# Optimization experiments

Measured on AMD Instinct MI355X. Metric: run time of the kernel, lower is better.

The kernel has to match this reference:

```python
import jax, jax.numpy as jnp
import numpy as np

D_MODEL = 1024
NUM_HEAD = 16
LN_EPS = 1e-5


def _layernorm(x, w, b):
    mu = jnp.mean(x, axis=-1, keepdims=True)
    var = jnp.mean(jnp.square(x - mu), axis=-1, keepdims=True)
    return (x - mu) * jax.lax.rsqrt(var + LN_EPS) * w + b


def setup_inputs() -> dict:
    key = jax.random.key(0)
    ks = jax.random.split(key, 8)
    d = D_MODEL
    s = 1.0 / np.sqrt(d)
    return {
        "text": jax.random.normal(ks[0], (8, 512, d), dtype=jnp.float32),
        "av_feat": jax.random.normal(ks[1], (8, 1024, d), dtype=jnp.float32),
        "tn_w": jnp.ones((d,), jnp.float32),
        "tn_b": jnp.zeros((d,), jnp.float32),
        "an_w": jnp.ones((d,), jnp.float32),
        "an_b": jnp.zeros((d,), jnp.float32),
        "Wq": jax.random.uniform(ks[2], (d, d), jnp.float32, -s, s),
        "bq": jnp.zeros((d,), jnp.float32),
        "Wk": jax.random.uniform(ks[3], (d, d), jnp.float32, -s, s),
        "bk": jnp.zeros((d,), jnp.float32),
        "Wv": jax.random.uniform(ks[4], (d, d), jnp.float32, -s, s),
        "bv": jnp.zeros((d,), jnp.float32),
    }


def reference(text, av_feat, tn_w, tn_b, an_w, an_b, Wq, bq, Wk, bk, Wv, bv):
    bs, num_word, d_model = text.shape
    num_valid = av_feat.shape[1]
    h = NUM_HEAD
    d_k = d_model // h

    t = _layernorm(text, tn_w, tn_b)
    a = _layernorm(av_feat, an_w, an_b)

    # torch Linear: x @ W.T + b
    q = (t @ Wq.T + bq).reshape(bs, num_word, h, d_k)   # b q h d
    k = (a @ Wk.T + bk).reshape(bs, num_valid, h, d_k)  # b k h d
    v = (a @ Wv.T + bv).reshape(bs, num_valid, h, d_k)  # b k h d

    # sigmoid attention (no softmax): scores (bs, num_word, num_valid, num_head)
    attn = jnp.einsum('bqhd,bkhd->bqkh', q, k) / np.sqrt(d_k)
    attn = jax.nn.sigmoid(attn)

    # out = sum over num_valid of attn * v -> (bs, num_word, num_head, d_k)
    out = jnp.einsum('bqkh,bkhd->bqhd', attn, v).reshape(bs, num_word, d_model)
    return out, attn.mean(-1)
```

## Files before the change

### kernel.cpp

```cpp
#include <hip/hip_runtime.h>
#include <hip/hip_bf16.h>

typedef float f32x4 __attribute__((ext_vector_type(4)));
typedef short s16x8 __attribute__((ext_vector_type(8)));

typedef const __attribute__((address_space(1))) unsigned int* gas1_t;
typedef __attribute__((address_space(3))) unsigned int* las3_t;

__device__ __forceinline__ void load_lds16(const void* g, void* l) {
  __builtin_amdgcn_global_load_lds((gas1_t)g, (las3_t)l, 16, 0, 0);
}

__device__ __forceinline__ unsigned short f2bf(float f) {
  union { float f; unsigned u; } v; v.f = f;
  unsigned u = v.u;
  u += 0x7fffu + ((u >> 16) & 1u);
  return (unsigned short)(u >> 16);
}
__device__ __forceinline__ float bf2f(unsigned short h) {
  union { unsigned u; float f; } v; v.u = ((unsigned)h) << 16;
  return v.f;
}

__global__ __launch_bounds__(256) void ln_bf16_kernel(
    const float* __restrict__ x, const float* __restrict__ w,
    const float* __restrict__ b, unsigned short* __restrict__ out) {
  int row = blockIdx.x;
  int tid = threadIdx.x;
  const float4* xr = (const float4*)(x + (size_t)row * 1024);
  float4 v = xr[tid];
  float s  = v.x + v.y + v.z + v.w;
  float ss = v.x * v.x + v.y * v.y + v.z * v.z + v.w * v.w;
  #pragma unroll
  for (int off = 32; off; off >>= 1) {
    s  += __shfl_down(s, off);
    ss += __shfl_down(ss, off);
  }
  __shared__ float red[8];
  int wid = tid >> 6, lane = tid & 63;
  if (lane == 0) { red[wid] = s; red[wid + 4] = ss; }
  __syncthreads();
  s  = red[0] + red[1] + red[2] + red[3];
  ss = red[4] + red[5] + red[6] + red[7];
  float mu  = s * (1.0f / 1024.0f);
  float var = ss * (1.0f / 1024.0f) - mu * mu;
  float rstd = rsqrtf(var + 1e-5f);
  float4 wv = ((const float4*)w)[tid];
  float4 bv = ((const float4*)b)[tid];
  ushort4 o;
  o.x = f2bf((v.x - mu) * rstd * wv.x + bv.x);
  o.y = f2bf((v.y - mu) * rstd * wv.y + bv.y);
  o.z = f2bf((v.z - mu) * rstd * wv.z + bv.z);
  o.w = f2bf((v.w - mu) * rstd * wv.w + bv.w);
  ((ushort4*)(out + (size_t)row * 1024))[tid] = o;
}

__global__ __launch_bounds__(256) void cvt_bf16_kernel(
    const float* __restrict__ in, unsigned short* __restrict__ out) {
  int i = blockIdx.x * 256 + threadIdx.x;
  float4 v = ((const float4*)in)[i];
  ushort4 o;
  o.x = f2bf(v.x); o.y = f2bf(v.y); o.z = f2bf(v.z); o.w = f2bf(v.w);
  ((ushort4*)out)[i] = o;
}

__global__ __launch_bounds__(256) void gemm_nt_bias_kernel(
    const unsigned short* __restrict__ A, const unsigned short* __restrict__ B,
    const float* __restrict__ bias, unsigned short* __restrict__ C, int M) {
  __shared__ unsigned short As[128 * 32];
  __shared__ unsigned short Bs[128 * 32];
  const int K = 1024, N = 1024;
  int tid = threadIdx.x, lane = tid & 63, wid = tid >> 6;
  int row0 = blockIdx.x * 128, col0 = blockIdx.y * 128;
  int wr = wid >> 1, wc = wid & 1;
  int l15 = lane & 15, kof = (lane >> 4) * 8;
  f32x4 acc[4][4] = {};
  for (int kt = 0; kt < K; kt += 32) {
    #pragma unroll
    for (int r = 0; r < 2; ++r) {
      int ch = wid * 64 + lane + r * 256;
      int rrow = ch >> 2, cc = ch & 3;
      load_lds16(&A[(size_t)(row0 + rrow) * K + kt + cc * 8], &As[ch * 8]);
      load_lds16(&B[(size_t)(col0 + rrow) * K + kt + cc * 8], &Bs[ch * 8]);
    }
    __syncthreads();
    s16x8 af[4], bfr[4];
    #pragma unroll
    for (int m = 0; m < 4; ++m)
      af[m] = *(const s16x8*)&As[(wr * 64 + m * 16 + l15) * 32 + kof];
    #pragma unroll
    for (int n = 0; n < 4; ++n)
      bfr[n] = *(const s16x8*)&Bs[(wc * 64 + n * 16 + l15) * 32 + kof];
    #pragma unroll
    for (int m = 0; m < 4; ++m)
      #pragma unroll
      for (int n = 0; n < 4; ++n)
        acc[m][n] = __builtin_amdgcn_mfma_f32_16x16x32_bf16(af[m], bfr[n], acc[m][n], 0, 0, 0);
    __syncthreads();
  }
  #pragma unroll
  for (int n = 0; n < 4; ++n) {
    int col = col0 + wc * 64 + n * 16 + l15;
    float bb = bias[col];
    #pragma unroll
    for (int m = 0; m < 4; ++m) {
      #pragma unroll
      for (int j = 0; j < 4; ++j) {
        int row = row0 + wr * 64 + m * 16 + (lane >> 4) * 4 + j;
        C[(size_t)row * N + col] = f2bf(acc[m][n][j] + bb);
      }
    }
  }
}

__global__ __launch_bounds__(1024, 4) void attn_kernel(
    const unsigned short* __restrict__ Q, const unsigned short* __restrict__ K,
    const unsigned short* __restrict__ V, float* __restrict__ out,
    float* __restrict__ meanout) {
  __shared__ unsigned short Klds[32 * 1024];
  __shared__ unsigned short Vlds[32 * 1024];
  __shared__ unsigned short Plds[16 * 16 * 32];
  int b = blockIdx.x >> 5, qt = blockIdx.x & 31;
  int q0 = qt * 16;
  int tid = threadIdx.x, lane = tid & 63, h = tid >> 6;
  int l15 = lane & 15, lg = lane >> 4;

  s16x8 aq0, aq1;
  {
    const unsigned short* qp = Q + (size_t)(b * 512 + q0 + l15) * 1024 + h * 64 + lg * 8;
    aq0 = *(const s16x8*)qp;
    aq1 = *(const s16x8*)(qp + 32);
  }
  f32x4 oacc[4] = {};

  for (int kt = 0; kt < 1024; kt += 32) {
    const unsigned short* Kg = K + (size_t)(b * 1024 + kt) * 1024;
    const unsigned short* Vg = V + (size_t)(b * 1024 + kt) * 1024;
    #pragma unroll
    for (int r = 0; r < 4; ++r) {
      int ch = tid + r * 1024;
      int key = ch >> 7, c = ch & 127;
      load_lds16(Kg + (size_t)key * 1024 + (size_t)((c ^ (key & 7)) * 8), &Klds[ch * 8]);
      load_lds16(Vg + (size_t)key * 1024 + (size_t)((c ^ ((key >> 3) << 1)) * 8), &Vlds[ch * 8]);
    }
    __syncthreads();

    f32x4 s0 = {}, s1 = {};
    #pragma unroll
    for (int ks = 0; ks < 2; ++ks) {
      int d = h * 64 + ks * 32 + lg * 8;
      int key0 = l15, key1 = 16 + l15;
      s16x8 bk0 = *(const s16x8*)&Klds[(key0 * 1024 + d) ^ ((key0 & 7) << 3)];
      s16x8 bk1 = *(const s16x8*)&Klds[(key1 * 1024 + d) ^ ((key1 & 7) << 3)];
      s16x8 aq = (ks == 0) ? aq0 : aq1;
      s0 = __builtin_amdgcn_mfma_f32_16x16x32_bf16(aq, bk0, s0, 0, 0, 0);
      s1 = __builtin_amdgcn_mfma_f32_16x16x32_bf16(aq, bk1, s1, 0, 0, 0);
    }
    #pragma unroll
    for (int j = 0; j < 4; ++j) {
      int q = lg * 4 + j;
      float p0 = 1.0f / (1.0f + __expf(-s0[j] * 0.125f));
      float p1 = 1.0f / (1.0f + __expf(-s1[j] * 0.125f));
      Plds[h * 512 + q * 32 + l15]      = f2bf(p0);
      Plds[h * 512 + q * 32 + 16 + l15] = f2bf(p1);
    }
    __syncthreads();

    if (tid < 512) {
      int q = tid >> 5, k = tid & 31;
      float sm = 0.f;
      #pragma unroll
      for (int hh = 0; hh < 16; ++hh) sm += bf2f(Plds[hh * 512 + q * 32 + k]);
      meanout[(size_t)(b * 512 + q0 + q) * 1024 + kt + k] = sm * 0.0625f;
    }

    s16x8 pa = *(const s16x8*)&Plds[h * 512 + l15 * 32 + lg * 8];
    #pragma unroll
    for (int nd = 0; nd < 4; ++nd) {
      int dcol = h * 64 + nd * 16 + l15;
      s16x8 bv;
      #pragma unroll
      for (int j = 0; j < 8; ++j) {
        int kk = lg * 8 + j;
        bv[j] = (short)Vlds[(kk * 1024 + dcol) ^ ((kk >> 3) << 4)];
      }
      oacc[nd] = __builtin_amdgcn_mfma_f32_16x16x32_bf16(pa, bv, oacc[nd], 0, 0, 0);
    }
    __syncthreads();
  }

  #pragma unroll
  for (int nd = 0; nd < 4; ++nd) {
    #pragma unroll
    for (int j = 0; j < 4; ++j) {
      int q = lg * 4 + j, d = h * 64 + nd * 16 + l15;
      out[(size_t)(b * 512 + q0 + q) * 1024 + d] = oacc[nd][j];
    }
  }
}

extern "C" void kernel_launch(void* const* d_in, const int* in_sizes, int n_in,
                              void* d_out, int out_size, void* d_ws, size_t ws_size,
                              hipStream_t stream) {
  const float* text = (const float*)d_in[0];
  const float* av   = (const float*)d_in[1];
  const float* tn_w = (const float*)d_in[2];
  const float* tn_b = (const float*)d_in[3];
  const float* an_w = (const float*)d_in[4];
  const float* an_b = (const float*)d_in[5];
  const float* Wq   = (const float*)d_in[6];
  const float* bq   = (const float*)d_in[7];
  const float* Wk   = (const float*)d_in[8];
  const float* bk   = (const float*)d_in[9];
  const float* Wv   = (const float*)d_in[10];
  const float* bv   = (const float*)d_in[11];

  char* ws = (char*)d_ws;
  const size_t MB = 1u << 20;
  unsigned short* Wqb = (unsigned short*)(ws + 0 * MB);
  unsigned short* Wkb = (unsigned short*)(ws + 2 * MB);
  unsigned short* Wvb = (unsigned short*)(ws + 4 * MB);
  unsigned short* Tln = (unsigned short*)(ws + 6 * MB);
  unsigned short* Aln = (unsigned short*)(ws + 14 * MB);
  unsigned short* Qb  = (unsigned short*)(ws + 30 * MB);
  unsigned short* Kb  = (unsigned short*)(ws + 38 * MB);
  unsigned short* Vb  = (unsigned short*)(ws + 54 * MB);

  float* out  = (float*)d_out;
  float* mout = out + (size_t)8 * 512 * 1024;

  ln_bf16_kernel<<<4096, 256, 0, stream>>>(text, tn_w, tn_b, Tln);
  ln_bf16_kernel<<<8192, 256, 0, stream>>>(av, an_w, an_b, Aln);
  cvt_bf16_kernel<<<1024, 256, 0, stream>>>(Wq, Wqb);
  cvt_bf16_kernel<<<1024, 256, 0, stream>>>(Wk, Wkb);
  cvt_bf16_kernel<<<1024, 256, 0, stream>>>(Wv, Wvb);
  dim3 gq(32, 8), gk(64, 8);
  gemm_nt_bias_kernel<<<gq, 256, 0, stream>>>(Tln, Wqb, bq, Qb, 4096);
  gemm_nt_bias_kernel<<<gk, 256, 0, stream>>>(Aln, Wkb, bk, Kb, 8192);
  gemm_nt_bias_kernel<<<gk, 256, 0, stream>>>(Aln, Wvb, bv, Vb, 8192);
  attn_kernel<<<8 * 32, 1024, 0, stream>>>(Qb, Kb, Vb, out, mout);
}
```

Before: 313.5 us.

## Transpose V in projection epilogue and read K/V directly from global in attention

The V projection GEMM now writes its output transposed per batch (d-major), so the attention kernel can load V fragments as contiguous 16-byte vectors straight from global memory. K staging through LDS is also dropped in favour of direct global loads. Each block now handles 32 queries instead of 16 with 128 blocks, and the P buffer uses a padded stride plus paired mean reads. This removes the large K/V LDS staging and the scalar strided V reads, at the cost of relying on cache for K/V reuse across heads. The grid is halved to 128 blocks, which may underfill the GPU.

```diff
diff --git a/kernel.cpp b/kernel.cpp
--- a/kernel.cpp
+++ b/kernel.cpp
@@ -16,10 +16,6 @@
   unsigned u = v.u;
   u += 0x7fffu + ((u >> 16) & 1u);
   return (unsigned short)(u >> 16);
-}
-__device__ __forceinline__ float bf2f(unsigned short h) {
-  union { unsigned u; float f; } v; v.u = ((unsigned)h) << 16;
-  return v.f;
 }
 
 __global__ __launch_bounds__(256) void ln_bf16_kernel(
@@ -64,6 +60,7 @@
   ((ushort4*)out)[i] = o;
 }
 
+template <int TRANS>
 __global__ __launch_bounds__(256) void gemm_nt_bias_kernel(
     const unsigned short* __restrict__ A, const unsigned short* __restrict__ B,
     const float* __restrict__ bias, unsigned short* __restrict__ C, int M) {
@@ -98,105 +95,136 @@
         acc[m][n] = __builtin_amdgcn_mfma_f32_16x16x32_bf16(af[m], bfr[n], acc[m][n], 0, 0, 0);
     __syncthreads();
   }
-  #pragma unroll
-  for (int n = 0; n < 4; ++n) {
-    int col = col0 + wc * 64 + n * 16 + l15;
-    float bb = bias[col];
-    #pragma unroll
-    for (int m = 0; m < 4; ++m) {
-      #pragma unroll
-      for (int j = 0; j < 4; ++j) {
-        int row = row0 + wr * 64 + m * 16 + (lane >> 4) * 4 + j;
-        C[(size_t)row * N + col] = f2bf(acc[m][n][j] + bb);
-      }
-    }
-  }
-}
-
+  int lg = lane >> 4;
+  if (TRANS) {
+    int b = row0 >> 10;
+    int kbase = (row0 & 1023) + wr * 64 + lg * 4;
+    #pragma unroll
+    for (int n = 0; n < 4; ++n) {
+      int col = col0 + wc * 64 + n * 16 + l15;
+      float bb = bias[col];
+      unsigned short* cp = C + (size_t)b * 1048576 + (size_t)col * 1024 + kbase;
+      #pragma unroll
+      for (int m = 0; m < 4; ++m) {
+        ushort4 o;
+        o.x = f2bf(acc[m][n][0] + bb);
+        o.y = f2bf(acc[m][n][1] + bb);
+        o.z = f2bf(acc[m][n][2] + bb);
+        o.w = f2bf(acc[m][n][3] + bb);
+        *(ushort4*)(cp + m * 16) = o;
+      }
+    }
+  } else {
+    #pragma unroll
+    for (int n = 0; n < 4; ++n) {
+      int col = col0 + wc * 64 + n * 16 + l15;
+      float bb = bias[col];
+      #pragma unroll
+      for (int m = 0; m < 4; ++m) {
+        #pragma unroll
+        for (int j = 0; j < 4; ++j) {
+          int row = row0 + wr * 64 + m * 16 + lg * 4 + j;
+          C[(size_t)row * N + col] = f2bf(acc[m][n][j] + bb);
+        }
+      }
+    }
+  }
+}
+
+#define PSTR 40
 __global__ __launch_bounds__(1024, 4) void attn_kernel(
     const unsigned short* __restrict__ Q, const unsigned short* __restrict__ K,
-    const unsigned short* __restrict__ V, float* __restrict__ out,
+    const unsigned short* __restrict__ Vt, float* __restrict__ out,
     float* __restrict__ meanout) {
-  __shared__ unsigned short Klds[32 * 1024];
-  __shared__ unsigned short Vlds[32 * 1024];
-  __shared__ unsigned short Plds[16 * 16 * 32];
-  int b = blockIdx.x >> 5, qt = blockIdx.x & 31;
-  int q0 = qt * 16;
+  __shared__ unsigned short Plds[16 * 32 * PSTR];
+  int bid = blockIdx.x;
+  int b = bid & 7, qt = bid >> 3;
+  int q0 = qt * 32;
   int tid = threadIdx.x, lane = tid & 63, h = tid >> 6;
   int l15 = lane & 15, lg = lane >> 4;
 
-  s16x8 aq0, aq1;
-  {
-    const unsigned short* qp = Q + (size_t)(b * 512 + q0 + l15) * 1024 + h * 64 + lg * 8;
-    aq0 = *(const s16x8*)qp;
-    aq1 = *(const s16x8*)(qp + 32);
-  }
-  f32x4 oacc[4] = {};
+  const unsigned short* Qp = Q + (size_t)(b * 512 + q0) * 1024 + h * 64;
+  const unsigned short* Kp = K + (size_t)b * 1048576 + h * 64;
+  const unsigned short* Vp = Vt + (size_t)b * 1048576 + (size_t)(h * 64) * 1024;
+
+  s16x8 aq[2][2];
+  #pragma unroll
+  for (int m = 0; m < 2; ++m)
+    #pragma unroll
+    for (int ks = 0; ks < 2; ++ks)
+      aq[m][ks] = *(const s16x8*)(Qp + (size_t)(m * 16 + l15) * 1024 + ks * 32 + lg * 8);
+
+  f32x4 oacc[2][4] = {};
+  unsigned short* Ph = Plds + h * (32 * PSTR);
 
   for (int kt = 0; kt < 1024; kt += 32) {
-    const unsigned short* Kg = K + (size_t)(b * 1024 + kt) * 1024;
-    const unsigned short* Vg = V + (size_t)(b * 1024 + kt) * 1024;
-    #pragma unroll
-    for (int r = 0; r < 4; ++r) {
-      int ch = tid + r * 1024;
-      int key = ch >> 7, c = ch & 127;
-      load_lds16(Kg + (size_t)key * 1024 + (size_t)((c ^ (key & 7)) * 8), &Klds[ch * 8]);
-      load_lds16(Vg + (size_t)key * 1024 + (size_t)((c ^ ((key >> 3) << 1)) * 8), &Vlds[ch * 8]);
-    }
-    __syncthreads();
-
-    f32x4 s0 = {}, s1 = {};
-    #pragma unroll
-    for (int ks = 0; ks < 2; ++ks) {
-      int d = h * 64 + ks * 32 + lg * 8;
-      int key0 = l15, key1 = 16 + l15;
-      s16x8 bk0 = *(const s16x8*)&Klds[(key0 * 1024 + d) ^ ((key0 & 7) << 3)];
-      s16x8 bk1 = *(const s16x8*)&Klds[(key1 * 1024 + d) ^ ((key1 & 7) << 3)];
-      s16x8 aq = (ks == 0) ? aq0 : aq1;
-      s0 = __builtin_amdgcn_mfma_f32_16x16x32_bf16(aq, bk0, s0, 0, 0, 0);
-      s1 = __builtin_amdgcn_mfma_f32_16x16x32_bf16(aq, bk1, s1, 0, 0, 0);
-    }
-    #pragma unroll
-    for (int j = 0; j < 4; ++j) {
-      int q = lg * 4 + j;
-      float p0 = 1.0f / (1.0f + __expf(-s0[j] * 0.125f));
-      float p1 = 1.0f / (1.0f + __expf(-s1[j] * 0.125f));
-      Plds[h * 512 + q * 32 + l15]      = f2bf(p0);
-      Plds[h * 512 + q * 32 + 16 + l15] = f2bf(p1);
-    }
+    f32x4 s[2][2] = {};
+    {
+      s16x8 bk[2][2];
+      #pragma unroll
+      for (int kc = 0; kc < 2; ++kc)
+        #pragma unroll
+        for (int ks = 0; ks < 2; ++ks)
+          bk[kc][ks] = *(const s16x8*)(Kp + (size_t)(kt + kc * 16 + l15) * 1024 + ks * 32 + lg * 8);
+      #pragma unroll
+      for (int m = 0; m < 2; ++m)
+        #pragma unroll
+        for (int kc = 0; kc < 2; ++kc) {
+          s[m][kc] = __builtin_amdgcn_mfma_f32_16x16x32_bf16(aq[m][0], bk[kc][0], s[m][kc], 0, 0, 0);
+          s[m][kc] = __builtin_amdgcn_mfma_f32_16x16x32_bf16(aq[m][1], bk[kc][1], s[m][kc], 0, 0, 0);
+        }
+    }
+    s16x8 bv[4];
+    #pragma unroll
+    for (int nd = 0; nd < 4; ++nd)
+      bv[nd] = *(const s16x8*)(Vp + (size_t)(nd * 16 + l15) * 1024 + kt + lg * 8);
+
+    #pragma unroll
+    for (int m = 0; m < 2; ++m)
+      #pragma unroll
+      for (int kc = 0; kc < 2; ++kc)
+        #pragma unroll
+        for (int j = 0; j < 4; ++j) {
+          float p = __builtin_amdgcn_rcpf(1.0f + __expf(s[m][kc][j] * -0.125f));
+          Ph[(m * 16 + lg * 4 + j) * PSTR + kc * 16 + l15] = f2bf(p);
+        }
     __syncthreads();
 
     if (tid < 512) {
-      int q = tid >> 5, k = tid & 31;
-      float sm = 0.f;
-      #pragma unroll
-      for (int hh = 0; hh < 16; ++hh) sm += bf2f(Plds[hh * 512 + q * 32 + k]);
-      meanout[(size_t)(b * 512 + q0 + q) * 1024 + kt + k] = sm * 0.0625f;
-    }
-
-    s16x8 pa = *(const s16x8*)&Plds[h * 512 + l15 * 32 + lg * 8];
-    #pragma unroll
-    for (int nd = 0; nd < 4; ++nd) {
-      int dcol = h * 64 + nd * 16 + l15;
-      s16x8 bv;
-      #pragma unroll
-      for (int j = 0; j < 8; ++j) {
-        int kk = lg * 8 + j;
-        bv[j] = (short)Vlds[(kk * 1024 + dcol) ^ ((kk >> 3) << 4)];
-      }
-      oacc[nd] = __builtin_amdgcn_mfma_f32_16x16x32_bf16(pa, bv, oacc[nd], 0, 0, 0);
-    }
+      int q = tid >> 4, kc2 = tid & 15;
+      const unsigned short* pp = Plds + q * PSTR + kc2 * 2;
+      float s0 = 0.f, s1 = 0.f;
+      #pragma unroll
+      for (int hh = 0; hh < 16; ++hh) {
+        unsigned u = *(const unsigned*)(pp + hh * (32 * PSTR));
+        union { unsigned u; float f; } lo, hi;
+        lo.u = u << 16; hi.u = u & 0xffff0000u;
+        s0 += lo.f; s1 += hi.f;
+      }
+      float2 mo; mo.x = s0 * 0.0625f; mo.y = s1 * 0.0625f;
+      *(float2*)&meanout[(size_t)(b * 512 + q0 + q) * 1024 + kt + kc2 * 2] = mo;
+    }
+
+    s16x8 pa[2];
+    pa[0] = *(const s16x8*)(Ph + l15 * PSTR + lg * 8);
+    pa[1] = *(const s16x8*)(Ph + (16 + l15) * PSTR + lg * 8);
+    #pragma unroll
+    for (int m = 0; m < 2; ++m)
+      #pragma unroll
+      for (int nd = 0; nd < 4; ++nd)
+        oacc[m][nd] = __builtin_amdgcn_mfma_f32_16x16x32_bf16(pa[m], bv[nd], oacc[m][nd], 0, 0, 0);
     __syncthreads();
   }
 
   #pragma unroll
-  for (int nd = 0; nd < 4; ++nd) {
-    #pragma unroll
-    for (int j = 0; j < 4; ++j) {
-      int q = lg * 4 + j, d = h * 64 + nd * 16 + l15;
-      out[(size_t)(b * 512 + q0 + q) * 1024 + d] = oacc[nd][j];
-    }
-  }
+  for (int m = 0; m < 2; ++m)
+    #pragma unroll
+    for (int nd = 0; nd < 4; ++nd)
+      #pragma unroll
+      for (int j = 0; j < 4; ++j) {
+        int q = m * 16 + lg * 4 + j, d = h * 64 + nd * 16 + l15;
+        out[(size_t)(b * 512 + q0 + q) * 1024 + d] = oacc[m][nd][j];
+      }
 }
 
 extern "C" void kernel_launch(void* const* d_in, const int* in_sizes, int n_in,
@@ -224,7 +252,7 @@
   unsigned short* Aln = (unsigned short*)(ws + 14 * MB);
   unsigned short* Qb  = (unsigned short*)(ws + 30 * MB);
   unsigned short* Kb  = (unsigned short*)(ws + 38 * MB);
-  unsigned short* Vb  = (unsigned short*)(ws + 54 * MB);
+  unsigned short* Vtb = (unsigned short*)(ws + 54 * MB);
 
   float* out  = (float*)d_out;
   float* mout = out + (size_t)8 * 512 * 1024;
@@ -235,8 +263,8 @@
   cvt_bf16_kernel<<<1024, 256, 0, stream>>>(Wk, Wkb);
   cvt_bf16_kernel<<<1024, 256, 0, stream>>>(Wv, Wvb);
   dim3 gq(32, 8), gk(64, 8);
-  gemm_nt_bias_kernel<<<gq, 256, 0, stream>>>(Tln, Wqb, bq, Qb, 4096);
-  gemm_nt_bias_kernel<<<gk, 256, 0, stream>>>(Aln, Wkb, bk, Kb, 8192);
-  gemm_nt_bias_kernel<<<gk, 256, 0, stream>>>(Aln, Wvb, bv, Vb, 8192);
-  attn_kernel<<<8 * 32, 1024, 0, stream>>>(Qb, Kb, Vb, out, mout);
-}
+  gemm_nt_bias_kernel<0><<<gq, 256, 0, stream>>>(Tln, Wqb, bq, Qb, 4096);
+  gemm_nt_bias_kernel<0><<<gk, 256, 0, stream>>>(Aln, Wkb, bk, Kb, 8192);
+  gemm_nt_bias_kernel<1><<<gk, 256, 0, stream>>>(Aln, Wvb, bv, Vtb, 8192);
+  attn_kernel<<<128, 1024, 0, stream>>>(Qb, Kb, Vtb, out, mout);
+}
```

Result: slower. 341.8 us (+9.0%).
